# Optimization experiments

Hardware: AMD Instinct MI355X
Metric: run time of the kernel (lower is better)

The kernel has to match this reference:

```python
import jax, jax.numpy as jnp
import numpy as np

B, S, DIM, H = 2, 2048, 1024, 16
HD = DIM // H

def setup_inputs() -> dict:
    key = jax.random.key(0)
    ks = jax.random.split(key, 11)
    sc = DIM ** -0.5
    return {
        "q": jax.random.normal(ks[0], (B, S, DIM), jnp.float32),
        "k": jax.random.normal(ks[1], (B, S, DIM), jnp.float32),
        "v": jax.random.normal(ks[2], (B, S, DIM), jnp.float32),
        "Wq": jax.random.normal(ks[3], (DIM, DIM), jnp.float32) * sc,
        "bq": jax.random.normal(ks[4], (DIM,), jnp.float32) * 0.02,
        "Wk": jax.random.normal(ks[5], (DIM, DIM), jnp.float32) * sc,
        "bk": jax.random.normal(ks[6], (DIM,), jnp.float32) * 0.02,
        "Wv": jax.random.normal(ks[7], (DIM, DIM), jnp.float32) * sc,
        "bv": jax.random.normal(ks[8], (DIM,), jnp.float32) * 0.02,
        "Wo": jax.random.normal(ks[9], (DIM, DIM), jnp.float32) * sc,
        "bo": jax.random.normal(ks[10], (DIM,), jnp.float32) * 0.02,
    }

def reference(q, k, v, Wq, bq, Wk, bk, Wv, bv, Wo, bo):
    b, s, _ = q.shape
    qh = (q @ Wq + bq).reshape(b, s, H, HD).transpose(0, 2, 1, 3)  # [B,H,S,HD]
    kh = (k @ Wk + bk).reshape(b, s, H, HD).transpose(0, 2, 1, 3)
    vh = (v @ Wv + bv).reshape(b, s, H, HD).transpose(0, 2, 1, 3)
    scale = HD ** -0.5
    scores = jnp.einsum('bhqd,bhkd->bhqk', qh, kh) * scale  # [B,H,S,S]
    causal = jnp.triu(jnp.ones((s, s), dtype=bool), k=1)
    scores = jnp.where(causal, -jnp.inf, scores)
    attn = jax.nn.softmax(scores, axis=-1)
    out = jnp.einsum('bhqk,bhkd->bhqd', attn, vh)
    out = out.transpose(0, 2, 1, 3).reshape(b, s, DIM)
    return out @ Wo + bo
```

## Files before the change

kernel.cpp:

```cpp
#include <hip/hip_runtime.h>

#define DIM 1024
#define SEQ 2048
#define NH 16
#define HD 64
#define M_TOT 4096

typedef unsigned short u16;
typedef unsigned int u32;
typedef __attribute__((ext_vector_type(8))) short bf16x8;
typedef __attribute__((ext_vector_type(4))) float f32x4;
typedef __attribute__((ext_vector_type(4))) u32 u32x4;
typedef __attribute__((ext_vector_type(4))) u16 u16x4;

__device__ __forceinline__ u16 f2bf(float f) {
  u32 x = __builtin_bit_cast(u32, f);
  x = x + 0x7fffu + ((x >> 16) & 1u);
  return (u16)(x >> 16);
}
__device__ __forceinline__ void gload_lds16(const void* g, void* l) {
  __builtin_amdgcn_global_load_lds(
      (const __attribute__((address_space(1))) u32*)g,
      (__attribute__((address_space(3))) u32*)l, 16, 0, 0);
}

__global__ __launch_bounds__(256)
void zero_out_k(u32* __restrict__ o, int n)
{
  int i = blockIdx.x * 256 + threadIdx.x;
  if (i < n) o[i] = 0;
}

__global__ __launch_bounds__(256)
void transpose_weights(const float* __restrict__ w0, const float* __restrict__ w1,
                       const float* __restrict__ w2, const float* __restrict__ w3,
                       u16* __restrict__ wt)
{
  __shared__ u16 tile[64][72];
  int z = blockIdx.z;
  const float* W = z == 0 ? w0 : z == 1 ? w1 : z == 2 ? w2 : w3;
  u16* Wt = wt + (size_t)z * DIM * DIM;
  int k0 = blockIdx.x * 64, n0 = blockIdx.y * 64;
  int t = threadIdx.x;
#pragma unroll
  for (int it = 0; it < 4; ++it) {
    int idx = it * 256 + t;
    int lr = idx >> 4, c0 = (idx & 15) * 4;
    f32x4 v = *(const f32x4*)&W[(size_t)(k0 + lr) * DIM + n0 + c0];
    u16x4 h;
#pragma unroll
    for (int j = 0; j < 4; ++j) h[j] = f2bf(v[j]);
    *(u16x4*)&tile[lr][c0] = h;
  }
  __syncthreads();
#pragma unroll
  for (int it = 0; it < 2; ++it) {
    int idx = it * 256 + t;
    int nr = idx >> 3, c0 = (idx & 7) * 8;
    alignas(16) u16 tmp[8];
#pragma unroll
    for (int j = 0; j < 8; ++j) tmp[j] = tile[c0 + j][nr];
    *(u32x4*)&Wt[(size_t)(n0 + nr) * DIM + k0 + c0] = *(u32x4*)tmp;
  }
}

#define BM 128
#define BN 128
#define BK 32

template <bool AF32, bool OUTF32>
__device__ __forceinline__ void gemm_tile(
    const void* __restrict__ Xv, const u16* __restrict__ Wt,
    const float* __restrict__ bias, void* __restrict__ Yv,
    int bm, int bn)
{
  __shared__ u16 lA[BM * BK];
  __shared__ u16 lB[BN * BK];
  int t = threadIdx.x;
  int lane = t & 63, w = t >> 6;
  int wr = (w >> 1) * 64, wc = (w & 1) * 64;
  int rl = lane & 15, kb = (lane >> 4) * 8;

  f32x4 acc[4][4] = {};

  for (int k0 = 0; k0 < DIM; k0 += BK) {
    if (AF32) {
      const float* Xf = (const float*)Xv;
#pragma unroll
      for (int it = 0; it < 4; ++it) {
        int idx = it * 256 + t;
        int row = idx >> 3, c4 = (idx & 7) * 4;
        f32x4 v = *(const f32x4*)&Xf[(size_t)(bm + row) * DIM + k0 + c4];
        u16x4 h;
#pragma unroll
        for (int j = 0; j < 4; ++j) h[j] = f2bf(v[j]);
        *(u16x4*)&lA[row * BK + c4] = h;
      }
    } else {
      const u16* Xh = (const u16*)Xv;
#pragma unroll
      for (int r = 0; r < 2; ++r) {
        int idx = r * 256 + t;
        int row = idx >> 2, ce = (idx & 3) * 8;
        gload_lds16(Xh + (size_t)(bm + row) * DIM + k0 + ce, (char*)lA + idx * 16);
      }
    }
#pragma unroll
    for (int r = 0; r < 2; ++r) {
      int idx = r * 256 + t;
      int row = idx >> 2, ce = (idx & 3) * 8;
      gload_lds16(Wt + (size_t)(bn + row) * DIM + k0 + ce, (char*)lB + idx * 16);
    }
    __syncthreads();
    bf16x8 a[4], b[4];
#pragma unroll
    for (int m = 0; m < 4; ++m)
      a[m] = *(const bf16x8*)&lA[(wr + m * 16 + rl) * BK + kb];
#pragma unroll
    for (int n = 0; n < 4; ++n)
      b[n] = *(const bf16x8*)&lB[(wc + n * 16 + rl) * BK + kb];
#pragma unroll
    for (int m = 0; m < 4; ++m)
#pragma unroll
      for (int n = 0; n < 4; ++n)
        acc[m][n] = __builtin_amdgcn_mfma_f32_16x16x32_bf16(a[m], b[n], acc[m][n], 0, 0, 0);
    __syncthreads();
  }

  int rh = (lane >> 4) * 4;
#pragma unroll
  for (int n = 0; n < 4; ++n) {
    int col = bn + wc + n * 16 + rl;
    float bv = bias[col];
#pragma unroll
    for (int m = 0; m < 4; ++m) {
      int row = bm + wr + m * 16 + rh;
#pragma unroll
      for (int r = 0; r < 4; ++r) {
        if (OUTF32)
          ((float*)Yv)[(size_t)(row + r) * DIM + col] = acc[m][n][r] + bv;
        else
          ((u16*)Yv)[(size_t)(row + r) * DIM + col] = f2bf(acc[m][n][r] + bv);
      }
    }
  }
}

__global__ __launch_bounds__(256)
void gemm_qkv(const float* __restrict__ xq, const float* __restrict__ xk, const float* __restrict__ xv,
              const u16* __restrict__ wt,
              const float* __restrict__ bq, const float* __restrict__ bk, const float* __restrict__ bv,
              u16* __restrict__ outbase)
{
  int z = blockIdx.z;
  const float* X = z == 0 ? xq : z == 1 ? xk : xv;
  const u16* Wt = wt + (size_t)z * DIM * DIM;
  const float* bias = z == 0 ? bq : z == 1 ? bk : bv;
  u16* Y = outbase + (size_t)z * M_TOT * DIM;
  gemm_tile<true, false>(X, Wt, bias, Y, blockIdx.x * BM, blockIdx.y * BN);
}

__global__ __launch_bounds__(256)
void gemm_o(const u16* __restrict__ X, const u16* __restrict__ Wt,
            const float* __restrict__ bias, float* __restrict__ Y)
{
  gemm_tile<false, true>(X, Wt, bias, Y, blockIdx.x * BM, blockIdx.y * BN);
}

__device__ __forceinline__ void attn_compute(
    const u16 (*lK)[72], const u16 (*lVt)[72], u16 (*lPw)[72],
    bf16x8 qf0, bf16x8 qf1, int rl, int hi, int kv0, int qw, bool diag,
    f32x4* oacc, float* mrow, float* lrow)
{
  float s[4][4];
#pragma unroll
  for (int g = 0; g < 4; ++g) {
    int kvr = g * 16 + rl;
    f32x4 c = {};
    c = __builtin_amdgcn_mfma_f32_16x16x32_bf16(qf0, *(const bf16x8*)&lK[kvr][hi * 8], c, 0, 0, 0);
    c = __builtin_amdgcn_mfma_f32_16x16x32_bf16(qf1, *(const bf16x8*)&lK[kvr][32 + hi * 8], c, 0, 0, 0);
#pragma unroll
    for (int r = 0; r < 4; ++r) s[g][r] = c[r] * 0.125f;
  }
  if (diag) {
#pragma unroll
    for (int g = 0; g < 4; ++g) {
      int kv_abs = kv0 + g * 16 + rl;
#pragma unroll
      for (int r = 0; r < 4; ++r)
        if (kv_abs > qw + hi * 4 + r) s[g][r] = -1e30f;
    }
  }
  float pm[4];
#pragma unroll
  for (int r = 0; r < 4; ++r)
    pm[r] = fmaxf(fmaxf(s[0][r], s[1][r]), fmaxf(s[2][r], s[3][r]));
#pragma unroll
  for (int mm = 1; mm <= 8; mm <<= 1)
#pragma unroll
    for (int r = 0; r < 4; ++r)
      pm[r] = fmaxf(pm[r], __shfl_xor(pm[r], mm));
  float fac[4], psum[4], p[4][4];
#pragma unroll
  for (int r = 0; r < 4; ++r) {
    float mn = fmaxf(mrow[r], pm[r]);
    fac[r] = __expf(mrow[r] - mn);
    mrow[r] = mn;
    psum[r] = 0.f;
  }
#pragma unroll
  for (int g = 0; g < 4; ++g)
#pragma unroll
    for (int r = 0; r < 4; ++r) {
      p[g][r] = __expf(s[g][r] - mrow[r]);
      psum[r] += p[g][r];
    }
#pragma unroll
  for (int mm = 1; mm <= 8; mm <<= 1)
#pragma unroll
    for (int r = 0; r < 4; ++r)
      psum[r] += __shfl_xor(psum[r], mm);
#pragma unroll
  for (int r = 0; r < 4; ++r) {
    lrow[r] = lrow[r] * fac[r] + psum[r];
#pragma unroll
    for (int n = 0; n < 4; ++n) oacc[n][r] *= fac[r];
  }
#pragma unroll
  for (int g = 0; g < 4; ++g)
#pragma unroll
    for (int r = 0; r < 4; ++r)
      lPw[hi * 4 + r][g * 16 + rl] = f2bf(p[g][r]);
#pragma unroll
  for (int kk = 0; kk < 2; ++kk) {
    bf16x8 pf = *(const bf16x8*)&lPw[rl][kk * 32 + hi * 8];
#pragma unroll
    for (int n = 0; n < 4; ++n) {
      bf16x8 vf = *(const bf16x8*)&lVt[n * 16 + rl][kk * 32 + hi * 8];
      oacc[n] = __builtin_amdgcn_mfma_f32_16x16x32_bf16(pf, vf, oacc[n], 0, 0, 0);
    }
  }
}

__global__ __launch_bounds__(256)
void attn_fwd(const u16* Qp, const u16* __restrict__ Kp,
              const u16* __restrict__ Vp, u16* O)
{
  __shared__ u16 lK[64][72];
  __shared__ u16 lVt[64][72];
  __shared__ u16 lP[4][16][72];

  int bh = blockIdx.y;
  int b = bh >> 4, h = bh & 15;
  int xa = blockIdx.x;
  int xb = 31 - xa;
  int t = threadIdx.x, lane = t & 63, w = t >> 6;
  int rl = lane & 15, hi = lane >> 4;
  int qa_w = xa * 64 + w * 16;
  int qb_w = xb * 64 + w * 16;

  const u16* Qb = Qp + ((size_t)b * SEQ) * DIM + h * HD;
  const u16* Kb = Kp + ((size_t)b * SEQ) * DIM + h * HD;
  const u16* Vb = Vp + ((size_t)b * SEQ) * DIM + h * HD;

  bf16x8 qa0, qa1, qb0, qb1;
  {
    const u16* qrow = Qb + (size_t)(qa_w + rl) * DIM + hi * 8;
    qa0 = *(const bf16x8*)qrow;
    qa1 = *(const bf16x8*)(qrow + 32);
    qrow = Qb + (size_t)(qb_w + rl) * DIM + hi * 8;
    qb0 = *(const bf16x8*)qrow;
    qb1 = *(const bf16x8*)(qrow + 32);
  }

  f32x4 oA[4] = {}, oB[4] = {};
  float mA[4], lA_[4], mB[4], lB_[4];
#pragma unroll
  for (int r = 0; r < 4; ++r) { mA[r] = mB[r] = -1e30f; lA_[r] = lB_[r] = 0.f; }

  int krow = t >> 3;
  int kc8 = (t & 7) * 8;
  int kvv = t & 63;
  int vd0 = (t >> 6) * 8;

  int nt = xb + 1;
  bf16x8 kr0, kr1, vr0, vr1;
  {
    const u16* Krow = Kb + kc8;
    kr0 = *(const bf16x8*)(Krow + (size_t)krow * DIM);
    kr1 = *(const bf16x8*)(Krow + (size_t)(krow + 32) * DIM);
    const u16* Vrow = Vb + (size_t)kvv * DIM + vd0;
    vr0 = *(const bf16x8*)Vrow;
    vr1 = *(const bf16x8*)(Vrow + 32);
  }

  for (int tile = 0; tile < nt; ++tile) {
    *(bf16x8*)&lK[krow][kc8] = kr0;
    *(bf16x8*)&lK[krow + 32][kc8] = kr1;
#pragma unroll
    for (int j = 0; j < 8; ++j) lVt[vd0 + j][kvv] = (u16)vr0[j];
#pragma unroll
    for (int j = 0; j < 8; ++j) lVt[vd0 + 32 + j][kvv] = (u16)vr1[j];
    __syncthreads();
    if (tile + 1 < nt) {
      int kv0n = (tile + 1) * 64;
      const u16* Krow = Kb + (size_t)kv0n * DIM + kc8;
      kr0 = *(const bf16x8*)(Krow + (size_t)krow * DIM);
      kr1 = *(const bf16x8*)(Krow + (size_t)(krow + 32) * DIM);
      const u16* Vrow = Vb + (size_t)(kv0n + kvv) * DIM + vd0;
      vr0 = *(const bf16x8*)Vrow;
      vr1 = *(const bf16x8*)(Vrow + 32);
    }
    int kv0 = tile * 64;
    attn_compute(lK, lVt, lP[w], qb0, qb1, rl, hi, kv0, qb_w, tile == xb, oB, mB, lB_);
    if (tile <= xa)
      attn_compute(lK, lVt, lP[w], qa0, qa1, rl, hi, kv0, qa_w, tile == xa, oA, mA, lA_);
    __syncthreads();
  }

#pragma unroll
  for (int n = 0; n < 4; ++n) {
    int d = n * 16 + rl;
#pragma unroll
    for (int r = 0; r < 4; ++r) {
      int qq = qa_w + hi * 4 + r;
      O[((size_t)b * SEQ + qq) * DIM + h * HD + d] = f2bf(oA[n][r] / lA_[r]);
      qq = qb_w + hi * 4 + r;
      O[((size_t)b * SEQ + qq) * DIM + h * HD + d] = f2bf(oB[n][r] / lB_[r]);
    }
  }
}

extern "C" void kernel_launch(void* const* d_in, const int* in_sizes, int n_in,
                              void* d_out, int out_size, void* d_ws, size_t ws_size,
                              hipStream_t stream)
{
  (void)in_sizes; (void)n_in;
  const size_t MB = 1024ull * 1024ull;
  if (ws_size < 32 * MB) {
    zero_out_k<<<(out_size + 255) / 256, 256, 0, stream>>>((u32*)d_out, out_size);
    return;
  }

  u16* Wt = (u16*)d_ws;
  u16* Qp = (u16*)((char*)d_ws + 8 * MB);
  u16* Kp = (u16*)((char*)d_ws + 16 * MB);
  u16* Vp = (u16*)((char*)d_ws + 24 * MB);

  transpose_weights<<<dim3(16, 16, 4), 256, 0, stream>>>(
      (const float*)d_in[3], (const float*)d_in[5], (const float*)d_in[7],
      (const float*)d_in[9], Wt);
  gemm_qkv<<<dim3(32, 8, 3), 256, 0, stream>>>(
      (const float*)d_in[0], (const float*)d_in[1], (const float*)d_in[2], Wt,
      (const float*)d_in[4], (const float*)d_in[6], (const float*)d_in[8], Qp);
  attn_fwd<<<dim3(16, 32), 256, 0, stream>>>(Qp, Kp, Vp, Qp);
  gemm_o<<<dim3(32, 8), 256, 0, stream>>>(Qp, Wt + 3ll * DIM * DIM,
                                          (const float*)d_in[10], (float*)d_out);
}
```

Before: 154.3 us.

## Double-buffer K/V tiles in LDS, fold softmax scale into exp2, add setprio

```diff
diff --git a/kernel.cpp b/kernel.cpp
--- a/kernel.cpp
+++ b/kernel.cpp
@@ -167,12 +167,15 @@
   gemm_tile<false, true>(X, Wt, bias, Y, blockIdx.x * BM, blockIdx.y * BN);
 }
 
+#define SC2 0.18033688011112042f
+
 __device__ __forceinline__ void attn_compute(
     const u16 (*lK)[72], const u16 (*lVt)[72], u16 (*lPw)[72],
     bf16x8 qf0, bf16x8 qf1, int rl, int hi, int kv0, int qw, bool diag,
     f32x4* oacc, float* mrow, float* lrow)
 {
   float s[4][4];
+  __builtin_amdgcn_s_setprio(1);
 #pragma unroll
   for (int g = 0; g < 4; ++g) {
     int kvr = g * 16 + rl;
@@ -180,8 +183,9 @@
     c = __builtin_amdgcn_mfma_f32_16x16x32_bf16(qf0, *(const bf16x8*)&lK[kvr][hi * 8], c, 0, 0, 0);
     c = __builtin_amdgcn_mfma_f32_16x16x32_bf16(qf1, *(const bf16x8*)&lK[kvr][32 + hi * 8], c, 0, 0, 0);
 #pragma unroll
-    for (int r = 0; r < 4; ++r) s[g][r] = c[r] * 0.125f;
-  }
+    for (int r = 0; r < 4; ++r) s[g][r] = c[r];
+  }
+  __builtin_amdgcn_s_setprio(0);
   if (diag) {
 #pragma unroll
     for (int g = 0; g < 4; ++g) {
@@ -203,8 +207,8 @@
   float fac[4], psum[4], p[4][4];
 #pragma unroll
   for (int r = 0; r < 4; ++r) {
-    float mn = fmaxf(mrow[r], pm[r]);
-    fac[r] = __expf(mrow[r] - mn);
+    float mn = fmaxf(mrow[r], pm[r] * SC2);
+    fac[r] = exp2f(mrow[r] - mn);
     mrow[r] = mn;
     psum[r] = 0.f;
   }
@@ -212,7 +216,7 @@
   for (int g = 0; g < 4; ++g)
 #pragma unroll
     for (int r = 0; r < 4; ++r) {
-      p[g][r] = __expf(s[g][r] - mrow[r]);
+      p[g][r] = exp2f(__builtin_fmaf(s[g][r], SC2, -mrow[r]));
       psum[r] += p[g][r];
     }
 #pragma unroll
@@ -231,6 +235,7 @@
 #pragma unroll
     for (int r = 0; r < 4; ++r)
       lPw[hi * 4 + r][g * 16 + rl] = f2bf(p[g][r]);
+  __builtin_amdgcn_s_setprio(1);
 #pragma unroll
   for (int kk = 0; kk < 2; ++kk) {
     bf16x8 pf = *(const bf16x8*)&lPw[rl][kk * 32 + hi * 8];
@@ -240,14 +245,15 @@
       oacc[n] = __builtin_amdgcn_mfma_f32_16x16x32_bf16(pf, vf, oacc[n], 0, 0, 0);
     }
   }
+  __builtin_amdgcn_s_setprio(0);
 }
 
 __global__ __launch_bounds__(256)
 void attn_fwd(const u16* Qp, const u16* __restrict__ Kp,
               const u16* __restrict__ Vp, u16* O)
 {
-  __shared__ u16 lK[64][72];
-  __shared__ u16 lVt[64][72];
+  __shared__ u16 lK[2][64][72];
+  __shared__ u16 lVt[2][64][72];
   __shared__ u16 lP[4][16][72];
 
   int bh = blockIdx.y;
@@ -292,30 +298,39 @@
     const u16* Vrow = Vb + (size_t)kvv * DIM + vd0;
     vr0 = *(const bf16x8*)Vrow;
     vr1 = *(const bf16x8*)(Vrow + 32);
+    *(bf16x8*)&lK[0][krow][kc8] = kr0;
+    *(bf16x8*)&lK[0][krow + 32][kc8] = kr1;
+#pragma unroll
+    for (int j = 0; j < 8; ++j) lVt[0][vd0 + j][kvv] = (u16)vr0[j];
+#pragma unroll
+    for (int j = 0; j < 8; ++j) lVt[0][vd0 + 32 + j][kvv] = (u16)vr1[j];
   }
 
   for (int tile = 0; tile < nt; ++tile) {
-    *(bf16x8*)&lK[krow][kc8] = kr0;
-    *(bf16x8*)&lK[krow + 32][kc8] = kr1;
-#pragma unroll
-    for (int j = 0; j < 8; ++j) lVt[vd0 + j][kvv] = (u16)vr0[j];
-#pragma unroll
-    for (int j = 0; j < 8; ++j) lVt[vd0 + 32 + j][kvv] = (u16)vr1[j];
+    int cur = tile & 1;
     __syncthreads();
     if (tile + 1 < nt) {
-      int kv0n = (tile + 1) * 64;
-      const u16* Krow = Kb + (size_t)kv0n * DIM + kc8;
+      size_t kv0n = (size_t)(tile + 1) * 64;
+      const u16* Krow = Kb + kv0n * DIM + kc8;
       kr0 = *(const bf16x8*)(Krow + (size_t)krow * DIM);
       kr1 = *(const bf16x8*)(Krow + (size_t)(krow + 32) * DIM);
-      const u16* Vrow = Vb + (size_t)(kv0n + kvv) * DIM + vd0;
+      const u16* Vrow = Vb + (kv0n + kvv) * DIM + vd0;
       vr0 = *(const bf16x8*)Vrow;
       vr1 = *(const bf16x8*)(Vrow + 32);
     }
     int kv0 = tile * 64;
-    attn_compute(lK, lVt, lP[w], qb0, qb1, rl, hi, kv0, qb_w, tile == xb, oB, mB, lB_);
+    attn_compute(lK[cur], lVt[cur], lP[w], qb0, qb1, rl, hi, kv0, qb_w, tile == xb, oB, mB, lB_);
     if (tile <= xa)
-      attn_compute(lK, lVt, lP[w], qa0, qa1, rl, hi, kv0, qa_w, tile == xa, oA, mA, lA_);
-    __syncthreads();
+      attn_compute(lK[cur], lVt[cur], lP[w], qa0, qa1, rl, hi, kv0, qa_w, tile == xa, oA, mA, lA_);
+    if (tile + 1 < nt) {
+      int nxt = cur ^ 1;
+      *(bf16x8*)&lK[nxt][krow][kc8] = kr0;
+      *(bf16x8*)&lK[nxt][krow + 32][kc8] = kr1;
+#pragma unroll
+      for (int j = 0; j < 8; ++j) lVt[nxt][vd0 + j][kvv] = (u16)vr0[j];
+#pragma unroll
+      for (int j = 0; j < 8; ++j) lVt[nxt][vd0 + 32 + j][kvv] = (u16)vr1[j];
+    }
   }
 
 #pragma unroll
```

Result: slower. 166.7 us (+8.0%).

## Split attention KV loop across two blocks and merge partials in combine kernel

Applied to the files above, without the earlier changes.

```diff
diff --git a/kernel.cpp b/kernel.cpp
--- a/kernel.cpp
+++ b/kernel.cpp
@@ -18,6 +18,10 @@
   x = x + 0x7fffu + ((x >> 16) & 1u);
   return (u16)(x >> 16);
 }
+__device__ __forceinline__ float bf2f(u16 u) {
+  u32 x = ((u32)u) << 16;
+  return __builtin_bit_cast(float, x);
+}
 __device__ __forceinline__ void gload_lds16(const void* g, void* l) {
   __builtin_amdgcn_global_load_lds(
       (const __attribute__((address_space(1))) u32*)g,
@@ -242,9 +246,10 @@
   }
 }
 
-__global__ __launch_bounds__(256)
-void attn_fwd(const u16* Qp, const u16* __restrict__ Kp,
-              const u16* __restrict__ Vp, u16* O)
+template <bool SPLIT>
+__device__ __forceinline__ void attn_body(
+    const u16* Qp, const u16* Kp, const u16* Vp, u16* O,
+    u16* Po, float* Pm, float* Pl)
 {
   __shared__ u16 lK[64][72];
   __shared__ u16 lVt[64][72];
@@ -254,6 +259,8 @@
   int b = bh >> 4, h = bh & 15;
   int xa = blockIdx.x;
   int xb = 31 - xa;
+  int z = SPLIT ? (int)blockIdx.z : 0;
+  int step = SPLIT ? 2 : 1;
   int t = threadIdx.x, lane = t & 63, w = t >> 6;
   int rl = lane & 15, hi = lane >> 4;
   int qa_w = xa * 64 + w * 16;
@@ -286,15 +293,16 @@
   int nt = xb + 1;
   bf16x8 kr0, kr1, vr0, vr1;
   {
-    const u16* Krow = Kb + kc8;
+    size_t kv00 = (size_t)z * 64;
+    const u16* Krow = Kb + kv00 * DIM + kc8;
     kr0 = *(const bf16x8*)(Krow + (size_t)krow * DIM);
     kr1 = *(const bf16x8*)(Krow + (size_t)(krow + 32) * DIM);
-    const u16* Vrow = Vb + (size_t)kvv * DIM + vd0;
+    const u16* Vrow = Vb + (kv00 + kvv) * DIM + vd0;
     vr0 = *(const bf16x8*)Vrow;
     vr1 = *(const bf16x8*)(Vrow + 32);
   }
 
-  for (int tile = 0; tile < nt; ++tile) {
+  for (int tile = z; tile < nt; tile += step) {
     *(bf16x8*)&lK[krow][kc8] = kr0;
     *(bf16x8*)&lK[krow + 32][kc8] = kr1;
 #pragma unroll
@@ -302,12 +310,12 @@
 #pragma unroll
     for (int j = 0; j < 8; ++j) lVt[vd0 + 32 + j][kvv] = (u16)vr1[j];
     __syncthreads();
-    if (tile + 1 < nt) {
-      int kv0n = (tile + 1) * 64;
-      const u16* Krow = Kb + (size_t)kv0n * DIM + kc8;
+    if (tile + step < nt) {
+      size_t kv0n = (size_t)(tile + step) * 64;
+      const u16* Krow = Kb + kv0n * DIM + kc8;
       kr0 = *(const bf16x8*)(Krow + (size_t)krow * DIM);
       kr1 = *(const bf16x8*)(Krow + (size_t)(krow + 32) * DIM);
-      const u16* Vrow = Vb + (size_t)(kv0n + kvv) * DIM + vd0;
+      const u16* Vrow = Vb + (kv0n + kvv) * DIM + vd0;
       vr0 = *(const bf16x8*)Vrow;
       vr1 = *(const bf16x8*)(Vrow + 32);
     }
@@ -318,17 +326,80 @@
     __syncthreads();
   }
 
-#pragma unroll
-  for (int n = 0; n < 4; ++n) {
-    int d = n * 16 + rl;
-#pragma unroll
-    for (int r = 0; r < 4; ++r) {
-      int qq = qa_w + hi * 4 + r;
-      O[((size_t)b * SEQ + qq) * DIM + h * HD + d] = f2bf(oA[n][r] / lA_[r]);
-      qq = qb_w + hi * 4 + r;
-      O[((size_t)b * SEQ + qq) * DIM + h * HD + d] = f2bf(oB[n][r] / lB_[r]);
-    }
-  }
+  if (!SPLIT) {
+#pragma unroll
+    for (int n = 0; n < 4; ++n) {
+      int d = n * 16 + rl;
+#pragma unroll
+      for (int r = 0; r < 4; ++r) {
+        int qq = qa_w + hi * 4 + r;
+        O[((size_t)b * SEQ + qq) * DIM + h * HD + d] = f2bf(oA[n][r] / lA_[r]);
+        qq = qb_w + hi * 4 + r;
+        O[((size_t)b * SEQ + qq) * DIM + h * HD + d] = f2bf(oB[n][r] / lB_[r]);
+      }
+    }
+  } else {
+    size_t zb = (size_t)z << 22;
+    int rbase = (bh << 11);
+#pragma unroll
+    for (int n = 0; n < 4; ++n) {
+      int d = n * 16 + rl;
+#pragma unroll
+      for (int r = 0; r < 4; ++r) {
+        int ra = rbase + qa_w + hi * 4 + r;
+        int rb = rbase + qb_w + hi * 4 + r;
+        Po[zb + (size_t)ra * 64 + d] = f2bf(oA[n][r]);
+        Po[zb + (size_t)rb * 64 + d] = f2bf(oB[n][r]);
+      }
+    }
+    if (rl == 0) {
+      int zo = z << 16;
+#pragma unroll
+      for (int r = 0; r < 4; ++r) {
+        int ra = rbase + qa_w + hi * 4 + r;
+        int rb = rbase + qb_w + hi * 4 + r;
+        Pm[zo + ra] = mA[r]; Pl[zo + ra] = lA_[r];
+        Pm[zo + rb] = mB[r]; Pl[zo + rb] = lB_[r];
+      }
+    }
+  }
+}
+
+__global__ __launch_bounds__(256)
+void attn_fwd(const u16* Qp, const u16* __restrict__ Kp,
+              const u16* __restrict__ Vp, u16* O)
+{
+  attn_body<false>(Qp, Kp, Vp, O, nullptr, nullptr, nullptr);
+}
+
+__global__ __launch_bounds__(256)
+void attn_fwd_split(const u16* Qp, const u16* __restrict__ Kp,
+                    const u16* __restrict__ Vp,
+                    u16* __restrict__ Po, float* __restrict__ Pm, float* __restrict__ Pl)
+{
+  attn_body<true>(Qp, Kp, Vp, nullptr, Po, Pm, Pl);
+}
+
+__global__ __launch_bounds__(256)
+void attn_combine(const u16* __restrict__ Po, const float* __restrict__ Pm,
+                  const float* __restrict__ Pl, u16* __restrict__ O)
+{
+  int gid = blockIdx.x * 256 + threadIdx.x;
+  int ridx = gid >> 3;
+  int d0 = (gid & 7) * 8;
+  float m0 = Pm[ridx], m1 = Pm[65536 + ridx];
+  float M = fmaxf(m0, m1);
+  float f0 = __expf(m0 - M), f1 = __expf(m1 - M);
+  float inv = 1.0f / (f0 * Pl[ridx] + f1 * Pl[65536 + ridx]);
+  bf16x8 a = *(const bf16x8*)(Po + (size_t)ridx * 64 + d0);
+  bf16x8 c = *(const bf16x8*)(Po + (1ull << 22) + (size_t)ridx * 64 + d0);
+  int bh = ridx >> 11, q = ridx & 2047;
+  int b = bh >> 4, h = bh & 15;
+  alignas(16) u16 tmp[8];
+#pragma unroll
+  for (int j = 0; j < 8; ++j)
+    tmp[j] = f2bf((f0 * bf2f((u16)a[j]) + f1 * bf2f((u16)c[j])) * inv);
+  *(u32x4*)(O + ((size_t)b * SEQ + q) * DIM + h * HD + d0) = *(u32x4*)tmp;
 }
 
 extern "C" void kernel_launch(void* const* d_in, const int* in_sizes, int n_in,
@@ -353,7 +424,16 @@
   gemm_qkv<<<dim3(32, 8, 3), 256, 0, stream>>>(
       (const float*)d_in[0], (const float*)d_in[1], (const float*)d_in[2], Wt,
       (const float*)d_in[4], (const float*)d_in[6], (const float*)d_in[8], Qp);
-  attn_fwd<<<dim3(16, 32), 256, 0, stream>>>(Qp, Kp, Vp, Qp);
+
+  if (ws_size >= 49 * MB) {
+    u16* Po = (u16*)((char*)d_ws + 32 * MB);
+    float* Pm = (float*)((char*)d_ws + 48 * MB);
+    float* Pl = (float*)((char*)d_ws + 48 * MB + 512 * 1024);
+    attn_fwd_split<<<dim3(16, 32, 2), 256, 0, stream>>>(Qp, Kp, Vp, Po, Pm, Pl);
+    attn_combine<<<2048, 256, 0, stream>>>(Po, Pm, Pl, Qp);
+  } else {
+    attn_fwd<<<dim3(16, 32), 256, 0, stream>>>(Qp, Kp, Vp, Qp);
+  }
   gemm_o<<<dim3(32, 8), 256, 0, stream>>>(Qp, Wt + 3ll * DIM * DIM,
                                           (const float*)d_in[10], (float*)d_out);
 }
```

Result: slower. 159.3 us (+3.2%).
